# Kernel optimization log

Measured on AMD Instinct MI355X. Metric: run time of the kernel, lower is better.

Reference implementation:

```python
import jax, jax.numpy as jnp
import numpy as np

N_ATOMS = 30000
N_PAIRS = 1200000
N_BASIS = 7
N_RADIAL = 5
N_SPECIES = 119
R_MIN = 0.5
R_MAX = 6.0
UNITS = (512, 512)
BOX = 6.0  # Angstrom box edge so many pairs fall inside the cutoff
N_FEAT = 360  # gaussian-moment feature count for n_radial=5

# static triangular index sets (fully symmetric contractions)
_TRI2_I, _TRI2_J = np.triu_indices(N_RADIAL)
_TRI3 = np.array([(i, j, k) for i in range(N_RADIAL)
                  for j in range(i, N_RADIAL)
                  for k in range(j, N_RADIAL)], dtype=np.int32)


def setup_inputs() -> dict:
    key = jax.random.key(0)
    ks = jax.random.split(key, 8)
    R = jax.random.uniform(ks[0], (N_ATOMS, 3), jnp.float32) * BOX
    Z = jax.random.randint(ks[1], (N_ATOMS,), 0, N_SPECIES, dtype=jnp.int32)
    idx = jax.random.randint(ks[2], (2, N_PAIRS), 0, N_ATOMS, dtype=jnp.int32)
    W_radial = jax.random.normal(ks[3], (N_SPECIES, N_SPECIES, N_RADIAL, N_BASIS), jnp.float32) / np.sqrt(N_BASIS)
    w1 = jax.random.normal(ks[4], (N_FEAT, UNITS[0]), jnp.float32) / np.sqrt(N_FEAT)
    b1 = jnp.zeros((UNITS[0],), jnp.float32)
    w2 = jax.random.normal(ks[5], (UNITS[0], UNITS[1]), jnp.float32) / np.sqrt(UNITS[0])
    b2 = jnp.zeros((UNITS[1],), jnp.float32)
    w3 = jax.random.normal(ks[6], (UNITS[1], 1), jnp.float32) / np.sqrt(UNITS[1])
    b3 = jnp.zeros((1,), jnp.float32)
    scale = 2.0 * jnp.ones((N_SPECIES, 1), jnp.float32)
    shift = 1.0 * jnp.ones((N_SPECIES, 1), jnp.float32)
    return dict(R=R, Z=Z, idx=idx, W_radial=W_radial, w1=w1, b1=b1,
                w2=w2, b2=b2, w3=w3, b3=b3, scale=scale, shift=shift)


def _descriptor(R, Z, idx, W_radial):
    idx_i, idx_j = idx[0], idx[1]
    # pairwise displacement (free-space displacement fn)
    dr_vec = R[idx_j] - R[idx_i]                                  # [P,3]
    dr = jnp.sqrt(jnp.sum(dr_vec * dr_vec, axis=-1) + 1e-12)      # [P]
    dn = dr_vec / (dr + 1e-5)[:, None]                            # unit vectors [P,3]

    # gaussian radial basis
    betta = N_BASIS ** 2 / R_MAX ** 2
    rad_norm = (2.0 * betta / np.pi) ** 0.25
    shifts = R_MIN + (R_MAX - R_MIN) / N_BASIS * jnp.arange(N_BASIS, dtype=jnp.float32)
    basis = rad_norm * jnp.exp(-betta * (dr[:, None] - shifts) ** 2)  # [P,B]

    # cosine cutoff and per species-pair embedding of the basis
    cutoff = 0.5 * (jnp.cos(jnp.pi * dr / R_MAX) + 1.0) * (dr < R_MAX)
    coeffs = W_radial[Z[idx_i], Z[idx_j]]                          # [P,K,B] irregular gather
    radial = jnp.einsum('pkb,pb->pk', coeffs, basis)               # [P,K]
    radial = radial * (cutoff / np.sqrt(N_BASIS))[:, None]

    seg = lambda x: jax.ops.segment_sum(x, idx_i, num_segments=N_ATOMS)
    # geometric moments of order 0..3
    m0 = seg(radial)                                               # [A,K]
    m1 = seg(radial[:, :, None] * dn[:, None, :])                  # [A,K,3]
    dn2 = dn[:, :, None] * dn[:, None, :]                          # [P,3,3]
    m2 = seg(radial[:, :, None, None] * dn2[:, None])              # [A,K,3,3]
    dn3 = dn2[:, :, :, None] * dn[:, None, None, :]                # [P,3,3,3]
    m3 = seg(radial[:, :, None, None, None] * dn3[:, None])        # [A,K,3,3,3]

    # gaussian-moment invariant contractions
    c1 = jnp.einsum('ari,asi->ars', m1, m1)
    c2 = jnp.einsum('arij,asij->ars', m2, m2)
    c3 = jnp.einsum('arijk,asijk->ars', m3, m3)
    c4 = jnp.einsum('arij,asik,atjk->arst', m2, m2, m2)
    c5 = jnp.einsum('ari,asj,atij->arst', m1, m1, m2)
    c6 = jnp.einsum('arijk,asijl,atkl->arst', m3, m3, m2)
    c7 = jnp.einsum('arijk,asij,atk->arst', m3, m2, m1)

    A = m0.shape[0]
    gm = jnp.concatenate([
        m0,
        c1[:, _TRI2_I, _TRI2_J],
        c2[:, _TRI2_I, _TRI2_J],
        c3[:, _TRI2_I, _TRI2_J],
        c4[:, _TRI3[:, 0], _TRI3[:, 1], _TRI3[:, 2]],
        c5[:, _TRI2_I, _TRI2_J, :].reshape(A, -1),
        c6[:, _TRI2_I, _TRI2_J, :].reshape(A, -1),
        c7.reshape(A, -1),
    ], axis=-1)                                                    # [A,360]
    return gm


def reference(R, Z, idx, W_radial, w1, b1, w2, b2, w3, b3, scale, shift):
    gm = _descriptor(R, Z, idx, W_radial)
    h = jax.nn.swish(gm @ w1 + b1)
    h = jax.nn.swish(h @ w2 + b2)
    h = h @ w3 + b3                                                # [A,1]
    return scale[Z] * h + shift[Z]
```

## Files before the change

### kernel.cpp

```cpp
#include <hip/hip_runtime.h>

#define NA      30000
#define MPAD    30080
#define NPAIRS  1200000
#define NB      7
#define NK      5
#define NSP     119
#define NFEAT   360
#define KP1     384
#define NU      512
#define WROW    36
#define MAXSLOT 120
#define PSTRIDE 128
#define NBK     118
#define BCAP    11520
#define PPB     4688
#define NTILE   235

#define BETTA      1.3611111111111112f
#define RADNORM    0.96481348f
#define SHIFT_STEP 0.7857142857142857f
#define PI_OVER_R  0.5235987755982988f
#define INV_SQRT7  0.3779644730092272f
#define RMAXV      6.0f

typedef __attribute__((ext_vector_type(8))) short bf16x8;
typedef __attribute__((ext_vector_type(4))) float f32x4;

__device__ __forceinline__ unsigned short f2b(float x) {
    unsigned u = __float_as_uint(x);
    unsigned r = u + 0x7FFF + ((u >> 16) & 1);
    return (unsigned short)(r >> 16);
}

__global__ __launch_bounds__(256)
void k_part(const int* __restrict__ idx, const int* __restrict__ Z,
            int* __restrict__ gcur, int* __restrict__ part) {
    __shared__ int hist[NBK];
    __shared__ int base[NBK];
    int tid = threadIdx.x;
    for (int b = tid; b < NBK; b += 256) hist[b] = 0;
    __syncthreads();
    int p0 = blockIdx.x * PPB;
    int p1 = min(p0 + PPB, NPAIRS);
    for (int p = p0 + tid; p < p1; p += 256)
        atomicAdd(&hist[idx[p] >> 8], 1);
    __syncthreads();
    for (int b = tid; b < NBK; b += 256) {
        base[b] = atomicAdd(&gcur[b], hist[b]);
        hist[b] = 0;
    }
    __syncthreads();
    for (int p = p0 + tid; p < p1; p += 256) {
        int i = idx[p];
        int b = i >> 8;
        int j = idx[NPAIRS + p];
        int zj = Z[j];
        int off = base[b] + atomicAdd(&hist[b], 1);
        if (off < BCAP)
            part[b * BCAP + off] = ((i & 255) << 22) | (zj << 15) | j;
    }
}

__global__ __launch_bounds__(256)
void k_csr(const int* __restrict__ part, const int* __restrict__ gcnt,
           int* __restrict__ counts, int* __restrict__ plist) {
    __shared__ int lp[128 * MAXSLOT];
    __shared__ int lc[128];
    int tid = threadIdx.x;
    int lane = tid & 63, wave = tid >> 6;
    int w = blockIdx.x;
    int cb = w >> 1;
    int par = w & 1;
    for (int t = tid; t < 128; t += 256) lc[t] = 0;
    __syncthreads();
    int n = min(gcnt[cb], BCAP);
    for (int e = tid; e < n; e += 256) {
        int v = part[cb * BCAP + e];
        int iloc = v >> 22;
        if ((iloc >> 7) == par) {
            int i7 = iloc & 127;
            int r = atomicAdd(&lc[i7], 1);
            if (r < MAXSLOT) lp[i7 * MAXSLOT + r] = v & 0x3FFFFF;
        }
    }
    __syncthreads();
    for (int t = tid; t < 128; t += 256) {
        int a = w * 128 + t;
        if (a < NA) counts[a] = min(lc[t], MAXSLOT);
    }
    for (int rr = 0; rr < 32; rr++) {
        int row = wave * 32 + rr;
        int a = w * 128 + row;
        if (a < NA) {
            for (int c = lane; c < MAXSLOT; c += 64)
                plist[(size_t)a * PSTRIDE + c] = lp[row * MAXSLOT + c];
        }
    }
}

#define PREP_W   (NSP*NSP*WROW)
#define PREP_R   NA
#define PREP_W1  (NU*KP1)
#define PREP_W2  (NU*NU)
#define PREP_TOT (PREP_W + PREP_R + PREP_W1 + PREP_W2)
__global__ void k_prep(const float* __restrict__ W, const float* __restrict__ R,
                       const float* __restrict__ w1, const float* __restrict__ w2,
                       float* __restrict__ Wp, float* __restrict__ Rp,
                       unsigned short* __restrict__ w1T, unsigned short* __restrict__ w2T) {
    int i = blockIdx.x * blockDim.x + threadIdx.x;
    if (i < PREP_W) {
        int row = i / WROW, e = i - row * WROW;
        Wp[i] = (e < NK * NB) ? W[row * (NK * NB) + e] : 0.f;
        return;
    }
    i -= PREP_W;
    if (i < PREP_R) {
        f32x4 v = {R[3*i], R[3*i+1], R[3*i+2], 0.f};
        *(f32x4*)&Rp[4*i] = v;
        return;
    }
    i -= PREP_R;
    if (i < PREP_W1) {
        int c = i / KP1, kp = i - c * KP1;
        w1T[i] = (kp < NFEAT) ? f2b(w1[kp * NU + c]) : (unsigned short)0;
        return;
    }
    i -= PREP_W1;
    if (i < PREP_W2) {
        int c = i >> 9, kp = i & 511;
        w2T[i] = f2b(w2[kp * NU + c]);
    }
}

__global__ __launch_bounds__(256, 2)
void k_moments(const float* __restrict__ Rp, const int* __restrict__ Z,
               const float* __restrict__ Wp,
               const int* __restrict__ counts,
               const int* __restrict__ plist, float* __restrict__ MT) {
    int tid = blockIdx.x * blockDim.x + threadIdx.x;
    int a = tid >> 3, q = tid & 7;
    if (a >= NA) return;
    f32x4 ri = *(const f32x4*)&Rp[4*a];
    int Zi = Z[a];
    float acc[100];
#pragma unroll
    for (int u = 0; u < 100; u++) acc[u] = 0.f;
    int cnt = min(counts[a], MAXSLOT);
    const int* prow = plist + (size_t)a * PSTRIDE;
    for (int t = q; t < cnt; t += 8) {
        int pk = prow[t];
        int j  = pk & 0x7FFF;
        int Zj = (pk >> 15) & 0x7F;
        f32x4 rj = *(const f32x4*)&Rp[4*j];
        float dx = rj.x - ri.x, dy = rj.y - ri.y, dz = rj.z - ri.z;
        float d2 = dx*dx + dy*dy + dz*dz + 1e-12f;
        float dr = sqrtf(d2);
        float inv = 1.0f / (dr + 1e-5f);
        float nx = dx*inv, ny = dy*inv, nz = dz*inv;

        const f32x4* wrow = (const f32x4*)&Wp[(Zi * NSP + Zj) * WROW];
        f32x4 w4[9];
#pragma unroll
        for (int c = 0; c < 9; c++) w4[c] = wrow[c];
        const float* wf = (const float*)w4;

        float basis[NB];
#pragma unroll
        for (int b = 0; b < NB; b++) {
            float tt = dr - (0.5f + SHIFT_STEP * (float)b);
            basis[b] = RADNORM * __expf(-BETTA * tt * tt);
        }
        float cut = (dr < RMAXV) ? 0.5f * (__cosf(PI_OVER_R * dr) + 1.0f) : 0.0f;
        cut *= INV_SQRT7;
        float rad[NK];
#pragma unroll
        for (int k = 0; k < NK; k++) {
            float s = 0.f;
#pragma unroll
            for (int b = 0; b < NB; b++) s += wf[k*NB + b] * basis[b];
            rad[k] = s * cut;
        }
        float g[20];
        g[0] = 1.f; g[1] = nx; g[2] = ny; g[3] = nz;
        g[4] = nx*nx; g[5] = nx*ny; g[6] = nx*nz; g[7] = ny*ny; g[8] = ny*nz; g[9] = nz*nz;
        g[10] = g[4]*nx; g[11] = g[4]*ny; g[12] = g[4]*nz; g[13] = g[5]*ny; g[14] = g[5]*nz;
        g[15] = g[6]*nz; g[16] = g[7]*ny; g[17] = g[7]*nz; g[18] = g[8]*nz; g[19] = g[9]*nz;
#pragma unroll
        for (int k = 0; k < NK; k++)
#pragma unroll
            for (int u = 0; u < 20; u++)
                acc[k*20 + u] += rad[k] * g[u];
    }
#pragma unroll
    for (int u = 0; u < 100; u++) {
        float v = acc[u];
        v += __shfl_xor(v, 1);
        v += __shfl_xor(v, 2);
        v += __shfl_xor(v, 4);
        acc[u] = v;
    }
    if (q == 0) {
#pragma unroll
        for (int u = 0; u < 100; u++) MT[u * NA + a] = acc[u];
    }
}

__global__ __launch_bounds__(256)
void k_contract(const float* __restrict__ MT, unsigned short* __restrict__ gmB) {
    __shared__ float M[100 * 64];
    int tid = threadIdx.x;
    int lane = tid & 63;
    int wave = tid >> 6;
    int a0 = blockIdx.x * 64;
    int a = a0 + lane;

    for (int e = tid; e < 6400; e += 256) {
        int u = e >> 6, l = e & 63;
        int aa = a0 + l;
        M[e] = (aa < NA) ? MT[u * NA + aa] : 0.f;
    }
    __syncthreads();

    const int S2[3][3] = {{0,1,2},{1,3,4},{2,4,5}};
    const int S3[3][3][3] = {
        {{0,1,2},{1,3,4},{2,4,5}},
        {{1,3,4},{3,6,7},{4,7,8}},
        {{2,4,5},{4,7,8},{5,8,9}}
    };
    bool ok = (a < NA);
    unsigned short* row = gmB + (size_t)a * KP1;
#define LD(comp) M[(comp) * 64 + lane]

    if (wave == 0) {
        if (ok) {
            for (int k = 0; k < 5; k++) row[k] = f2b(LD(k * 20));
        }
        int f = 5;
        for (int r = 0; r < 5; r++)
            for (int s = r; s < 5; s++) {
                float v = 0.f;
#pragma unroll
                for (int i = 0; i < 3; i++) v += LD(r*20+1+i) * LD(s*20+1+i);
                if (ok) row[f] = f2b(v);
                f++;
            }
        const float W2U[6] = {1,2,2,1,2,1};
        for (int r = 0; r < 5; r++)
            for (int s = r; s < 5; s++) {
                float v = 0.f;
#pragma unroll
                for (int u = 0; u < 6; u++) v += W2U[u] * LD(r*20+4+u) * LD(s*20+4+u);
                if (ok) row[f] = f2b(v);
                f++;
            }
        const float W3U[10] = {1,3,3,3,6,3,1,3,3,1};
        for (int r = 0; r < 5; r++)
            for (int s = r; s < 5; s++) {
                float v = 0.f;
#pragma unroll
                for (int u = 0; u < 10; u++) v += W3U[u] * LD(r*20+10+u) * LD(s*20+10+u);
                if (ok) row[f] = f2b(v);
                f++;
            }
        for (int r = 0; r < 5; r++) {
            float m2r[6];
#pragma unroll
            for (int u = 0; u < 6; u++) m2r[u] = LD(r*20+4+u);
            for (int s = r; s < 5; s++) {
                float m2q[6];
#pragma unroll
                for (int u = 0; u < 6; u++) m2q[u] = LD(s*20+4+u);
                for (int t = s; t < 5; t++) {
                    float m2t[6];
#pragma unroll
                    for (int u = 0; u < 6; u++) m2t[u] = LD(t*20+4+u);
                    float v = 0.f;
#pragma unroll
                    for (int i = 0; i < 3; i++)
#pragma unroll
                        for (int j = 0; j < 3; j++)
#pragma unroll
                            for (int k = 0; k < 3; k++)
                                v += m2r[S2[i][j]] * m2q[S2[i][k]] * m2t[S2[j][k]];
                    if (ok) row[f] = f2b(v);
                    f++;
                }
            }
        }
    } else if (wave == 1) {
        int f = 85;
        for (int r = 0; r < 5; r++) {
            float m1r[3];
#pragma unroll
            for (int i = 0; i < 3; i++) m1r[i] = LD(r*20+1+i);
            for (int s = r; s < 5; s++) {
                float m1q[3];
#pragma unroll
                for (int i = 0; i < 3; i++) m1q[i] = LD(s*20+1+i);
                for (int t = 0; t < 5; t++) {
                    float m2t[6];
#pragma unroll
                    for (int u = 0; u < 6; u++) m2t[u] = LD(t*20+4+u);
                    float v = 0.f;
#pragma unroll
                    for (int i = 0; i < 3; i++)
#pragma unroll
                        for (int j = 0; j < 3; j++)
                            v += m1r[i] * m1q[j] * m2t[S2[i][j]];
                    if (ok) row[f] = f2b(v);
                    f++;
                }
            }
        }
        f = 235;
        for (int r = 0; r < 5; r++) {
            float m3r[10];
#pragma unroll
            for (int u = 0; u < 10; u++) m3r[u] = LD(r*20+10+u);
            for (int s = 0; s < 5; s++) {
                float m2q[6];
#pragma unroll
                for (int u = 0; u < 6; u++) m2q[u] = LD(s*20+4+u);
                float U0 = 0.f, U1 = 0.f, U2 = 0.f;
#pragma unroll
                for (int i = 0; i < 3; i++)
#pragma unroll
                    for (int j = 0; j < 3; j++) {
                        float ww = m2q[S2[i][j]];
                        U0 += m3r[S3[i][j][0]] * ww;
                        U1 += m3r[S3[i][j][1]] * ww;
                        U2 += m3r[S3[i][j][2]] * ww;
                    }
                for (int t = 0; t < 5; t++) {
                    float v = U0 * LD(t*20+1) + U1 * LD(t*20+2) + U2 * LD(t*20+3);
                    if (ok) row[f] = f2b(v);
                    f++;
                }
            }
        }
    } else {
        int pbeg = (wave == 2) ? 0 : 7;
        int pend = (wave == 2) ? 7 : 15;
        int p = 0;
        for (int r = 0; r < 5; r++)
            for (int s = r; s < 5; s++) {
                if (p >= pbeg && p < pend) {
                    float m3r[10], m3q[10];
#pragma unroll
                    for (int u = 0; u < 10; u++) m3r[u] = LD(r*20+10+u);
#pragma unroll
                    for (int u = 0; u < 10; u++) m3q[u] = LD(s*20+10+u);
                    float T[3][3];
#pragma unroll
                    for (int k = 0; k < 3; k++)
#pragma unroll
                        for (int l = 0; l < 3; l++) {
                            float v = 0.f;
#pragma unroll
                            for (int i = 0; i < 3; i++)
#pragma unroll
                                for (int j = 0; j < 3; j++)
                                    v += m3r[S3[i][j][k]] * m3q[S3[i][j][l]];
                            T[k][l] = v;
                        }
                    int f = 160 + p * 5;
                    for (int t = 0; t < 5; t++) {
                        float m2t[6];
#pragma unroll
                        for (int u = 0; u < 6; u++) m2t[u] = LD(t*20+4+u);
                        float v = 0.f;
#pragma unroll
                        for (int k = 0; k < 3; k++)
#pragma unroll
                            for (int l = 0; l < 3; l++)
                                v += T[k][l] * m2t[S2[k][l]];
                        if (ok) row[f + t] = f2b(v);
                    }
                }
                p++;
            }
        if (wave == 3 && ok) {
            for (int z = NFEAT; z < KP1; z++) row[z] = 0;
        }
    }
#undef LD
}

__device__ __forceinline__ void stage8(const unsigned short* gp, unsigned short* lp) {
    __builtin_amdgcn_global_load_lds(
        (const __attribute__((address_space(1))) unsigned int*)gp,
        (__attribute__((address_space(3))) unsigned int*)lp, 16, 0, 0);
}

template<int KPAD, int MODE>
__global__ __launch_bounds__(256) void k_mfma(const unsigned short* __restrict__ A,
                                              const unsigned short* __restrict__ B,
                                              const float* __restrict__ bias,
                                              const float* __restrict__ w3,
                                              void* __restrict__ outp) {
    __shared__ __align__(16) unsigned char SMEM[35072];
    unsigned short* As = (unsigned short*)SMEM;
    unsigned short* Bs = (unsigned short*)(SMEM + 16384);
    float* red = (float*)(SMEM + 32768);
    int tid = threadIdx.x;
    int lane = tid & 63, wave = tid >> 6;
    int wm = wave >> 1, wn = wave & 1;
    int quad = lane >> 4, l16 = lane & 15;
    int lrow = lane >> 3;
    int lchk = lane & 7;

    for (int t = 0; t < 2; t++) {
        int atile = blockIdx.y * 2 + t;
        if (atile >= NTILE) break;
        int rowA0, rowB0;
        if (MODE == 1) { rowA0 = atile * 128;      rowB0 = blockIdx.x * 128; }
        else           { rowA0 = blockIdx.x * 128; rowB0 = atile * 128; }

        f32x4 acc[4][4];
        f32x4 zero = {0.f, 0.f, 0.f, 0.f};
#pragma unroll
        for (int i = 0; i < 4; i++)
#pragma unroll
            for (int j = 0; j < 4; j++) acc[i][j] = zero;

        for (int k0 = 0; k0 < KPAD; k0 += 64) {
            __syncthreads();
#pragma unroll
            for (int i = 0; i < 4; i++) {
                int r = wave * 32 + i * 8 + lrow;
                int gc = lchk ^ (r & 7);
                stage8(A + (size_t)(rowA0 + r) * KPAD + k0 + gc * 8, &As[(wave * 32 + i * 8) * 64]);
            }
#pragma unroll
            for (int i = 0; i < 4; i++) {
                int r = wave * 32 + i * 8 + lrow;
                int gc = lchk ^ (r & 7);
                stage8(B + (size_t)(rowB0 + r) * KPAD + k0 + gc * 8, &Bs[(wave * 32 + i * 8) * 64]);
            }
            __syncthreads();
#pragma unroll
            for (int s = 0; s < 2; s++) {
                bf16x8 af[4], bfr[4];
#pragma unroll
                for (int mt = 0; mt < 4; mt++) {
                    int r = wm * 64 + mt * 16 + l16;
                    af[mt] = *(const bf16x8*)&As[r * 64 + (((s * 4 + quad) ^ (r & 7)) * 8)];
                }
#pragma unroll
                for (int nt = 0; nt < 4; nt++) {
                    int r = wn * 64 + nt * 16 + l16;
                    bfr[nt] = *(const bf16x8*)&Bs[r * 64 + (((s * 4 + quad) ^ (r & 7)) * 8)];
                }
#pragma unroll
                for (int mt = 0; mt < 4; mt++)
#pragma unroll
                    for (int nt = 0; nt < 4; nt++)
                        acc[mt][nt] = __builtin_amdgcn_mfma_f32_16x16x32_bf16(
                            af[mt], bfr[nt], acc[mt][nt], 0, 0, 0);
            }
        }

        if (MODE == 1) {
            __syncthreads();
            unsigned short* Ot = (unsigned short*)SMEM;
#pragma unroll
            for (int nt = 0; nt < 4; nt++) {
                int c_loc = wn * 64 + nt * 16 + l16;
                float b = bias[rowB0 + c_loc];
#pragma unroll
                for (int mt = 0; mt < 4; mt++) {
#pragma unroll
                    for (int reg = 0; reg < 4; reg++) {
                        int a_loc = wm * 64 + mt * 16 + quad * 4 + reg;
                        float v = acc[mt][nt][reg] + b;
                        Ot[a_loc * 136 + c_loc] = f2b(v / (1.f + __expf(-v)));
                    }
                }
            }
            __syncthreads();
            unsigned short* O = (unsigned short*)outp;
            int half = lane >> 5, l32 = lane & 31;
#pragma unroll
            for (int it = 0; it < 16; it++) {
                int rloc = wave * 32 + it * 2 + half;
                int a = rowA0 + rloc;
                unsigned long long d = *(const unsigned long long*)&Ot[rloc * 136 + l32 * 4];
                if (a < NA)
                    *(unsigned long long*)&O[(size_t)a * NU + rowB0 + l32 * 4] = d;
            }
        } else {
            float pn[4] = {0.f, 0.f, 0.f, 0.f};
#pragma unroll
            for (int mt = 0; mt < 4; mt++) {
#pragma unroll
                for (int reg = 0; reg < 4; reg++) {
                    int c = rowA0 + wm * 64 + mt * 16 + quad * 4 + reg;
                    float b = bias[c];
                    float w3c = w3[c];
#pragma unroll
                    for (int nt = 0; nt < 4; nt++) {
                        float v = acc[mt][nt][reg] + b;
                        pn[nt] += w3c * (v / (1.f + __expf(-v)));
                    }
                }
            }
#pragma unroll
            for (int nt = 0; nt < 4; nt++) {
                pn[nt] += __shfl_xor(pn[nt], 16);
                pn[nt] += __shfl_xor(pn[nt], 32);
            }
            __syncthreads();
            if (quad == 0) {
#pragma unroll
                for (int nt = 0; nt < 4; nt++)
                    red[((wm * 2 + wn) * 4 + nt) * 16 + l16] = pn[nt];
            }
            __syncthreads();
            if (tid < 128) {
                int wn2 = tid >> 6, nt2 = (tid >> 4) & 3, lb = tid & 15;
                float s = red[((0 * 2 + wn2) * 4 + nt2) * 16 + lb]
                        + red[((1 * 2 + wn2) * 4 + nt2) * 16 + lb];
                int a = rowB0 + wn2 * 64 + nt2 * 16 + lb;
                if (a < NA) atomicAdd((float*)outp + a, s);
            }
        }
    }
}

__global__ void k_finish(float* __restrict__ out, const float* __restrict__ b3,
                         const int* __restrict__ Z, const float* __restrict__ scale,
                         const float* __restrict__ shift) {
    int a = blockIdx.x * blockDim.x + threadIdx.x;
    if (a >= NA) return;
    int z = Z[a];
    out[a] = scale[z] * (out[a] + b3[0]) + shift[z];
}

extern "C" void kernel_launch(void* const* d_in, const int* in_sizes, int n_in,
                              void* d_out, int out_size, void* d_ws, size_t ws_size,
                              hipStream_t stream) {
    const float* R    = (const float*)d_in[0];
    const int*   Z    = (const int*)  d_in[1];
    const int*   idx  = (const int*)  d_in[2];
    const float* Wr   = (const float*)d_in[3];
    const float* w1   = (const float*)d_in[4];
    const float* b1   = (const float*)d_in[5];
    const float* w2   = (const float*)d_in[6];
    const float* b2   = (const float*)d_in[7];
    const float* w3   = (const float*)d_in[8];
    const float* b3   = (const float*)d_in[9];
    const float* scale= (const float*)d_in[10];
    const float* shift= (const float*)d_in[11];
    float* out = (float*)d_out;
    char* ws = (char*)d_ws;

    int*            gcur   = (int*)  (ws + 0);
    int*            counts = (int*)  (ws + 512);
    int*            part   = (int*)  (ws + 120576);
    int*            plist  = (int*)  (ws + 5558016);
    float*          MT     = (float*)(ws + 20918016);
    unsigned short* gmB    = (unsigned short*)(ws + 32918016);
    unsigned short* w1T    = (unsigned short*)(ws + 56019456);
    unsigned short* w2T    = (unsigned short*)(ws + 56412672);
    unsigned short* h1B    = (unsigned short*)(ws + 56936960);
    float*          Wpad   = (float*)(ws + 87738880);
    float*          Rpad   = (float*)(ws + 89778064);

    hipMemsetAsync(gcur, 0, 512, stream);
    hipMemsetAsync(d_out, 0, NA * sizeof(float), stream);

    k_part    <<<256, 256, 0, stream>>>(idx, Z, gcur, part);
    k_csr     <<<235, 256, 0, stream>>>(part, gcur, counts, plist);
    k_prep    <<<(PREP_TOT + 255) / 256, 256, 0, stream>>>(Wr, R, w1, w2, Wpad, Rpad, w1T, w2T);
    k_moments <<<(NA * 8 + 255) / 256, 256, 0, stream>>>(Rpad, Z, Wpad, counts, plist, MT);
    k_contract<<<(NA + 63) / 64,       256, 0, stream>>>(MT, gmB);

    k_mfma<KP1, 1><<<dim3(NU / 128, 118), 256, 0, stream>>>(gmB, w1T, b1, nullptr, (void*)h1B);
    k_mfma<NU,  2><<<dim3(NU / 128, 118), 256, 0, stream>>>(w2T, h1B, b2, w3, (void*)out);

    k_finish<<<(NA + 255) / 256, 256, 0, stream>>>(out, b3, Z, scale, shift);
}
```

Baseline: 271.0 us.

## Fuse moment accumulation and invariant contraction into one kernel via LDS

Merges k_moments and k_contract so that each block handles 16 atoms. Each atom is served by 16 threads instead of 8. The 100 moment components stay in shared memory and are contracted there, and the bf16 features are staged in LDS before coalesced writes to gmB. This drops the MT global round trip and one kernel launch. In exchange, only 16 of 64 lanes in each wave do contraction work, and the MAXSLOT clamp on the pair count is removed.

```diff
diff --git a/kernel.cpp b/kernel.cpp
--- a/kernel.cpp
+++ b/kernel.cpp
@@ -135,36 +135,40 @@
 
 __global__ __launch_bounds__(256, 2)
 void k_moments(const float* __restrict__ Rp, const int* __restrict__ Z,
-               const float* __restrict__ Wp,
-               const int* __restrict__ counts,
-               const int* __restrict__ plist, float* __restrict__ MT) {
-    int tid = blockIdx.x * blockDim.x + threadIdx.x;
-    int a = tid >> 3, q = tid & 7;
-    if (a >= NA) return;
+               const float* __restrict__ Wp, const int* __restrict__ counts,
+               const int* __restrict__ plist, unsigned short* __restrict__ gmB) {
+    __shared__ float MS[100 * 17];
+    __shared__ unsigned short FS[16 * 392];
+    int tid = threadIdx.x;
+    int g = tid >> 4, q = tid & 15;
+    int a0 = blockIdx.x * 16;
+    int a = a0 + g;
     f32x4 ri = *(const f32x4*)&Rp[4*a];
     int Zi = Z[a];
     float acc[100];
 #pragma unroll
     for (int u = 0; u < 100; u++) acc[u] = 0.f;
-    int cnt = min(counts[a], MAXSLOT);
+    int cnt = counts[a];
     const int* prow = plist + (size_t)a * PSTRIDE;
-    for (int t = q; t < cnt; t += 8) {
+
+    for (int t = q; t < cnt; t += 16) {
         int pk = prow[t];
         int j  = pk & 0x7FFF;
         int Zj = (pk >> 15) & 0x7F;
         f32x4 rj = *(const f32x4*)&Rp[4*j];
+
+        const f32x4* wrow = (const f32x4*)&Wp[(Zi * NSP + Zj) * WROW];
+        f32x4 w4[9];
+#pragma unroll
+        for (int c = 0; c < 9; c++) w4[c] = wrow[c];
+        const float* wf = (const float*)w4;
+
         float dx = rj.x - ri.x, dy = rj.y - ri.y, dz = rj.z - ri.z;
         float d2 = dx*dx + dy*dy + dz*dz + 1e-12f;
         float dr = sqrtf(d2);
         float inv = 1.0f / (dr + 1e-5f);
         float nx = dx*inv, ny = dy*inv, nz = dz*inv;
 
-        const f32x4* wrow = (const f32x4*)&Wp[(Zi * NSP + Zj) * WROW];
-        f32x4 w4[9];
-#pragma unroll
-        for (int c = 0; c < 9; c++) w4[c] = wrow[c];
-        const float* wf = (const float*)w4;
-
         float basis[NB];
 #pragma unroll
         for (int b = 0; b < NB; b++) {
@@ -181,16 +185,16 @@
             for (int b = 0; b < NB; b++) s += wf[k*NB + b] * basis[b];
             rad[k] = s * cut;
         }
-        float g[20];
-        g[0] = 1.f; g[1] = nx; g[2] = ny; g[3] = nz;
-        g[4] = nx*nx; g[5] = nx*ny; g[6] = nx*nz; g[7] = ny*ny; g[8] = ny*nz; g[9] = nz*nz;
-        g[10] = g[4]*nx; g[11] = g[4]*ny; g[12] = g[4]*nz; g[13] = g[5]*ny; g[14] = g[5]*nz;
-        g[15] = g[6]*nz; g[16] = g[7]*ny; g[17] = g[7]*nz; g[18] = g[8]*nz; g[19] = g[9]*nz;
+        float gg[20];
+        gg[0] = 1.f; gg[1] = nx; gg[2] = ny; gg[3] = nz;
+        gg[4] = nx*nx; gg[5] = nx*ny; gg[6] = nx*nz; gg[7] = ny*ny; gg[8] = ny*nz; gg[9] = nz*nz;
+        gg[10] = gg[4]*nx; gg[11] = gg[4]*ny; gg[12] = gg[4]*nz; gg[13] = gg[5]*ny; gg[14] = gg[5]*nz;
+        gg[15] = gg[6]*nz; gg[16] = gg[7]*ny; gg[17] = gg[7]*nz; gg[18] = gg[8]*nz; gg[19] = gg[9]*nz;
 #pragma unroll
         for (int k = 0; k < NK; k++)
 #pragma unroll
             for (int u = 0; u < 20; u++)
-                acc[k*20 + u] += rad[k] * g[u];
+                acc[k*20 + u] += rad[k] * gg[u];
     }
 #pragma unroll
     for (int u = 0; u < 100; u++) {
@@ -198,43 +202,30 @@
         v += __shfl_xor(v, 1);
         v += __shfl_xor(v, 2);
         v += __shfl_xor(v, 4);
+        v += __shfl_xor(v, 8);
         acc[u] = v;
     }
     if (q == 0) {
 #pragma unroll
-        for (int u = 0; u < 100; u++) MT[u * NA + a] = acc[u];
-    }
-}
-
-__global__ __launch_bounds__(256)
-void k_contract(const float* __restrict__ MT, unsigned short* __restrict__ gmB) {
-    __shared__ float M[100 * 64];
-    int tid = threadIdx.x;
-    int lane = tid & 63;
-    int wave = tid >> 6;
-    int a0 = blockIdx.x * 64;
-    int a = a0 + lane;
-
-    for (int e = tid; e < 6400; e += 256) {
-        int u = e >> 6, l = e & 63;
-        int aa = a0 + l;
-        M[e] = (aa < NA) ? MT[u * NA + aa] : 0.f;
-    }
-    __syncthreads();
-
+        for (int u = 0; u < 100; u++) MS[u * 17 + g] = acc[u];
+    }
+    __syncthreads();
+
+    int lane = tid & 63, wave = tid >> 6;
+    int g16 = lane & 15;
+    bool act = lane < 16;
     const int S2[3][3] = {{0,1,2},{1,3,4},{2,4,5}};
     const int S3[3][3][3] = {
         {{0,1,2},{1,3,4},{2,4,5}},
         {{1,3,4},{3,6,7},{4,7,8}},
         {{2,4,5},{4,7,8},{5,8,9}}
     };
-    bool ok = (a < NA);
-    unsigned short* row = gmB + (size_t)a * KP1;
-#define LD(comp) M[(comp) * 64 + lane]
+    unsigned short* frow = &FS[g16 * 392];
+#define LD(comp) MS[(comp) * 17 + g16]
 
     if (wave == 0) {
-        if (ok) {
-            for (int k = 0; k < 5; k++) row[k] = f2b(LD(k * 20));
+        if (act) {
+            for (int k = 0; k < 5; k++) frow[k] = f2b(LD(k * 20));
         }
         int f = 5;
         for (int r = 0; r < 5; r++)
@@ -242,7 +233,7 @@
                 float v = 0.f;
 #pragma unroll
                 for (int i = 0; i < 3; i++) v += LD(r*20+1+i) * LD(s*20+1+i);
-                if (ok) row[f] = f2b(v);
+                if (act) frow[f] = f2b(v);
                 f++;
             }
         const float W2U[6] = {1,2,2,1,2,1};
@@ -251,7 +242,7 @@
                 float v = 0.f;
 #pragma unroll
                 for (int u = 0; u < 6; u++) v += W2U[u] * LD(r*20+4+u) * LD(s*20+4+u);
-                if (ok) row[f] = f2b(v);
+                if (act) frow[f] = f2b(v);
                 f++;
             }
         const float W3U[10] = {1,3,3,3,6,3,1,3,3,1};
@@ -260,7 +251,7 @@
                 float v = 0.f;
 #pragma unroll
                 for (int u = 0; u < 10; u++) v += W3U[u] * LD(r*20+10+u) * LD(s*20+10+u);
-                if (ok) row[f] = f2b(v);
+                if (act) frow[f] = f2b(v);
                 f++;
             }
         for (int r = 0; r < 5; r++) {
@@ -283,7 +274,7 @@
 #pragma unroll
                             for (int k = 0; k < 3; k++)
                                 v += m2r[S2[i][j]] * m2q[S2[i][k]] * m2t[S2[j][k]];
-                    if (ok) row[f] = f2b(v);
+                    if (act) frow[f] = f2b(v);
                     f++;
                 }
             }
@@ -308,7 +299,7 @@
 #pragma unroll
                         for (int j = 0; j < 3; j++)
                             v += m1r[i] * m1q[j] * m2t[S2[i][j]];
-                    if (ok) row[f] = f2b(v);
+                    if (act) frow[f] = f2b(v);
                     f++;
                 }
             }
@@ -334,7 +325,7 @@
                     }
                 for (int t = 0; t < 5; t++) {
                     float v = U0 * LD(t*20+1) + U1 * LD(t*20+2) + U2 * LD(t*20+3);
-                    if (ok) row[f] = f2b(v);
+                    if (act) frow[f] = f2b(v);
                     f++;
                 }
             }
@@ -375,16 +366,22 @@
 #pragma unroll
                             for (int l = 0; l < 3; l++)
                                 v += T[k][l] * m2t[S2[k][l]];
-                        if (ok) row[f + t] = f2b(v);
+                        if (act) frow[f + t] = f2b(v);
                     }
                 }
                 p++;
             }
-        if (wave == 3 && ok) {
-            for (int z = NFEAT; z < KP1; z++) row[z] = 0;
+        if (wave == 3 && act) {
+            for (int z = NFEAT; z < KP1; z++) frow[z] = 0;
         }
     }
 #undef LD
+    __syncthreads();
+    for (int e = tid; e < 16 * KP1; e += 256) {
+        int at = e / KP1;
+        int f = e - at * KP1;
+        gmB[(size_t)(a0 + at) * KP1 + f] = FS[at * 392 + f];
+    }
 }
 
 __device__ __forceinline__ void stage8(const unsigned short* gp, unsigned short* lp) {
@@ -559,7 +556,6 @@
     int*            counts = (int*)  (ws + 512);
     int*            part   = (int*)  (ws + 120576);
     int*            plist  = (int*)  (ws + 5558016);
-    float*          MT     = (float*)(ws + 20918016);
     unsigned short* gmB    = (unsigned short*)(ws + 32918016);
     unsigned short* w1T    = (unsigned short*)(ws + 56019456);
     unsigned short* w2T    = (unsigned short*)(ws + 56412672);
@@ -573,8 +569,7 @@
     k_part    <<<256, 256, 0, stream>>>(idx, Z, gcur, part);
     k_csr     <<<235, 256, 0, stream>>>(part, gcur, counts, plist);
     k_prep    <<<(PREP_TOT + 255) / 256, 256, 0, stream>>>(Wr, R, w1, w2, Wpad, Rpad, w1T, w2T);
-    k_moments <<<(NA * 8 + 255) / 256, 256, 0, stream>>>(Rpad, Z, Wpad, counts, plist, MT);
-    k_contract<<<(NA + 63) / 64,       256, 0, stream>>>(MT, gmB);
+    k_moments <<<NA / 16, 256, 0, stream>>>(Rpad, Z, Wpad, counts, plist, gmB);
 
     k_mfma<KP1, 1><<<dim3(NU / 128, 118), 256, 0, stream>>>(gmB, w1T, b1, nullptr, (void*)h1B);
     k_mfma<NU,  2><<<dim3(NU / 128, 118), 256, 0, stream>>>(w2T, h1B, b2, w3, (void*)out);
```

Result: slower. 289.5 us (+6.8%).
